# Optimization experiments

Measured on AMD Instinct MI355X. Metric: run time of the kernel, lower is better.

Reference implementation:

```python
import jax, jax.numpy as jnp
import numpy as np

HIDDEN = 2560
NUM_HEADS = 32
HEAD = HIDDEN // NUM_HEADS  # 80
ROT = 32                    # partial rotary dim (phi)
THETA = 10000.0
B, S = 2, 2048


def _apply_rope(x, pos):
    """Neox-style rotary embedding on the first ROT dims of the head.
    x: [B, S, H, HEAD], pos: [B, S] int."""
    inv_freq = 1.0 / (THETA ** (jnp.arange(0, ROT, 2, dtype=jnp.float32) / ROT))  # [ROT/2]
    freqs = pos.astype(jnp.float32)[..., None] * inv_freq  # [B, S, ROT/2]
    cos = jnp.cos(freqs)[:, :, None, :].astype(x.dtype)    # [B, S, 1, ROT/2]
    sin = jnp.sin(freqs)[:, :, None, :].astype(x.dtype)
    x_rot, x_pass = x[..., :ROT], x[..., ROT:]
    x1, x2 = x_rot[..., :ROT // 2], x_rot[..., ROT // 2:]
    rotated = jnp.concatenate([x1 * cos - x2 * sin, x2 * cos + x1 * sin], axis=-1)
    return jnp.concatenate([rotated, x_pass], axis=-1)


def setup_inputs() -> dict:
    key = jax.random.key(0)
    k0, k1, k2 = jax.random.split(key, 3)
    hidden_states = jax.random.normal(k0, (B, S, HIDDEN), dtype=jnp.float32)
    position_ids = jnp.broadcast_to(jnp.arange(S, dtype=jnp.int32), (B, S))
    Wqkv_w = jax.random.normal(k1, (3 * HIDDEN, HIDDEN), dtype=jnp.float32) * 0.02
    Wqkv_b = jnp.zeros((3 * HIDDEN,), dtype=jnp.float32)
    out_w = jax.random.normal(k2, (HIDDEN, HIDDEN), dtype=jnp.float32) * 0.02
    out_b = jnp.zeros((HIDDEN,), dtype=jnp.float32)
    return {"position_ids": position_ids, "hidden_states": hidden_states,
            "Wqkv_w": Wqkv_w, "Wqkv_b": Wqkv_b, "out_w": out_w, "out_b": out_b}


def reference(position_ids, hidden_states, Wqkv_w, Wqkv_b, out_w, out_b):
    # Fused QKV projection (torch Linear: y = x @ W^T + b)
    qkv = jnp.einsum('bsh,oh->bso', hidden_states, Wqkv_w) + Wqkv_b  # [B,S,3*HIDDEN]
    q, k, v = jnp.split(qkv, 3, axis=-1)
    q = q.reshape(B, S, NUM_HEADS, HEAD)
    k = k.reshape(B, S, NUM_HEADS, HEAD)
    v = v.reshape(B, S, NUM_HEADS, HEAD)
    # Inline RoPE on q/k (partial, first ROT dims)
    q = _apply_rope(q, position_ids)
    k = _apply_rope(k, position_ids)
    # Causal scaled-dot-product attention (math of the paged prefill kernel)
    scale = HEAD ** -0.5
    scores = jnp.einsum('bqhd,bkhd->bhqk', q, k) * scale  # [B,H,S,S]
    causal = jnp.tril(jnp.ones((S, S), dtype=bool))
    scores = jnp.where(causal, scores, jnp.finfo(scores.dtype).min)
    attn = jax.nn.softmax(scores, axis=-1)
    ctx = jnp.einsum('bhqk,bkhd->bqhd', attn, v).reshape(B, S, HIDDEN)
    return jnp.einsum('bsh,oh->bso', ctx, out_w) + out_b
```

## Files before the change

### kernel.cpp

```cpp
#include <hip/hip_runtime.h>
#include <stdint.h>

#define HIDDEN  2560
#define NHEADS  32
#define HEAD    80
#define QKS     96
#define SEQ     2048
#define BATCH   2
#define M_TOTAL (BATCH*SEQ)
#define QKV_N   (3*HIDDEN)
#define PART_SLOTS 36

typedef __attribute__((ext_vector_type(8))) short  short8;
typedef __attribute__((ext_vector_type(4))) float  floatx4;
typedef __attribute__((ext_vector_type(4))) float  fvec4;
typedef __attribute__((ext_vector_type(4))) unsigned short usvec4;
typedef __attribute__((ext_vector_type(2))) unsigned int uint2v;

#define SBAR() __builtin_amdgcn_sched_barrier(0)

__device__ __forceinline__ unsigned short f2bf(float x){
  union { float f; unsigned u; } v; v.f = x;
  unsigned r = v.u + 0x7fffu + ((v.u >> 16) & 1u);
  return (unsigned short)(r >> 16);
}
__device__ __forceinline__ float bf2f(unsigned short h){
  union { unsigned u; float f; } v; v.u = ((unsigned)h) << 16;
  return v.f;
}
__device__ __forceinline__ unsigned cvt_pk_bf16(float lo, float hi){
  unsigned r;
  asm volatile("v_cvt_pk_bf16_f32 %0, %1, %2" : "=v"(r) : "v"(lo), "v"(hi));
  return r;
}
__device__ __forceinline__ void gload16(const void* g, void* l){
  __builtin_amdgcn_global_load_lds(
    (const __attribute__((address_space(1))) void*)g,
    (__attribute__((address_space(3))) void*)l, 16, 0, 0);
}

__global__ __launch_bounds__(256)
void convert_f32_bf16(const float* __restrict__ src, unsigned short* __restrict__ dst, int n4){
  int idx = blockIdx.x*blockDim.x + threadIdx.x;
  int stride = gridDim.x*blockDim.x;
  for (int i = idx; i < n4; i += stride){
    fvec4 v = *(const fvec4*)(src + (size_t)i*4);
    usvec4 o;
    o[0]=f2bf(v[0]); o[1]=f2bf(v[1]); o[2]=f2bf(v[2]); o[3]=f2bf(v[3]);
    *(usvec4*)(dst + (size_t)i*4) = o;
  }
}

template<bool OUT_BF16>
__global__ __launch_bounds__(512, 2)
void gemm256(const unsigned short* __restrict__ A, const unsigned short* __restrict__ Bm,
             const float* __restrict__ bias, void* __restrict__ Cout,
             int M, int N, int K)
{
  __shared__ __align__(16) unsigned short lds[65536];
  const int tid  = threadIdx.x;
  const int lane = tid & 63;
  const int w    = tid >> 6;
  const int wm   = w >> 2;
  const int wn   = w & 3;
  const int l15  = lane & 15, lg = lane >> 4;

  const int gx  = gridDim.x;
  const int lid = blockIdx.y*gx + blockIdx.x;
  const int nwg = gx*gridDim.y;
  const int qch = nwg >> 3;
  const int sl  = (lid & 7)*qch + (lid >> 3);
  const int bn0 = (sl % gx) * 256;
  const int bm0 = (sl / gx) * 256;

  const int nt = K >> 6;

  int rowq[2], cq[2];
  #pragma unroll
  for (int q=0;q<2;q++){
    int u = (w*2+q)*64 + lane;
    rowq[q] = u >> 2;
    cq[q]   = ((u & 3) - (rowq[q] >> 1)) & 3;
  }
  const int rot = (lg + (l15 >> 1)) & 3;

  floatx4 acc[8][4];
  #pragma unroll
  for (int m=0;m<8;m++)
    #pragma unroll
    for (int n=0;n<4;n++) acc[m][n] = (floatx4)0.0f;

  auto STAGE = [&](int tau, int kkh){
    const int bufb = tau & 1;
    const size_t kofs = (size_t)tau*64 + kkh*32;
    const unsigned sA = (unsigned)(((bufb*2 + 0)*2 + kkh) * 8192);
    const unsigned sB = (unsigned)(((bufb*2 + 1)*2 + kkh) * 8192);
    #pragma unroll
    for (int q=0;q<2;q++){
      gload16(A  + (size_t)(bm0 + rowq[q])*K + kofs + cq[q]*8, &lds[sA + (w*2+q)*512]);
      gload16(Bm + (size_t)(bn0 + rowq[q])*K + kofs + cq[q]*8, &lds[sB + (w*2+q)*512]);
    }
  };
  auto COMPUTE = [&](int bufb, int kkh){
    const unsigned short* As = &lds[((bufb*2+0)*2+kkh)*8192];
    const unsigned short* Bs = &lds[((bufb*2+1)*2+kkh)*8192];
    short8 af[8], bfv[4];
    __builtin_amdgcn_s_setprio(1);
    #pragma unroll
    for (int n=0;n<4;n++)
      bfv[n] = *(const short8*)&Bs[(((wn*64 + n*16 + l15)<<2) + rot)*8];
    #pragma unroll
    for (int m=0;m<8;m++)
      af[m] = *(const short8*)&As[(((wm*128 + m*16 + l15)<<2) + rot)*8];
    #pragma unroll
    for (int m=0;m<8;m++)
      #pragma unroll
      for (int n=0;n<4;n++)
        acc[m][n] = __builtin_amdgcn_mfma_f32_16x16x32_bf16(af[m], bfv[n], acc[m][n], 0, 0, 0);
    __builtin_amdgcn_s_setprio(0);
  };

  STAGE(0,0);
  STAGE(0,1);
  STAGE(1,0);
  asm volatile("s_waitcnt vmcnt(8)" ::: "memory");
  __builtin_amdgcn_s_barrier(); SBAR();

  for (int t=0; t<nt; ++t){
    const int c = t & 1;
    if (t+1 < nt) STAGE(t+1, 1);
    COMPUTE(c, 0);
    if (t+1 < nt) asm volatile("s_waitcnt vmcnt(8)" ::: "memory");
    else          asm volatile("s_waitcnt vmcnt(0)" ::: "memory");
    __builtin_amdgcn_s_barrier(); SBAR();
    if (t+2 < nt) STAGE(t+2, 0);
    COMPUTE(c, 1);
    if (t+1 < nt){
      if (t+2 < nt) asm volatile("s_waitcnt vmcnt(8)" ::: "memory");
      else          asm volatile("s_waitcnt vmcnt(4)" ::: "memory");
      __builtin_amdgcn_s_barrier(); SBAR();
    }
  }

  #pragma unroll
  for (int m=0;m<8;m++){
    #pragma unroll
    for (int n=0;n<4;n++){
      int col = bn0 + wn*64 + n*16 + l15;
      float bs = bias[col];
      #pragma unroll
      for (int r=0;r<4;r++){
        int row = bm0 + wm*128 + m*16 + lg*4 + r;
        float v = acc[m][n][r] + bs;
        if (OUT_BF16) ((unsigned short*)Cout)[(size_t)row*N + col] = f2bf(v);
        else          ((float*)Cout)[(size_t)row*N + col] = v;
      }
    }
  }
}

__global__ __launch_bounds__(256)
void rope_scatter(const unsigned short* __restrict__ qkv,
                  const int* __restrict__ pos_ids,
                  unsigned short* __restrict__ Qp, unsigned short* __restrict__ Kp,
                  unsigned short* __restrict__ Vt)
{
  __shared__ float cosb[128*16];
  __shared__ float sinb[128*16];
  __shared__ __align__(16) unsigned short vtile[128*88];
  const int tid = threadIdx.x;
  const int blk = blockIdx.x;
  const int st = blk & 15, h = (blk >> 4) & 31, b = blk >> 9;
  const int s0 = st*128;

  for (int idx = tid; idx < 128*16; idx += 256){
    int sl = idx >> 4, i = idx & 15;
    float p = (float)pos_ids[b*SEQ + s0 + sl];
    float inv = exp2f(-(float)i * (13.287712379549449f/16.0f));
    float ang = p * inv;
    cosb[idx] = cosf(ang);
    sinb[idx] = sinf(ang);
  }
  __syncthreads();

  const size_t qkrow = (size_t)(b*SEQ + s0)*QKV_N;
  const size_t obase = ((size_t)(b*NHEADS + h)*SEQ + s0)*QKS;
  #pragma unroll
  for (int part = 0; part < 2; part++){
    const int cbase = part*HIDDEN + h*HEAD;
    unsigned short* outp = part ? Kp : Qp;
    for (int idx = tid; idx < 128*QKS; idx += 256){
      int sl = idx / QKS, d = idx - sl*QKS;
      const size_t rb = qkrow + (size_t)sl*QKV_N + cbase;
      float v;
      if (d < 16){
        float x1 = bf2f(qkv[rb + d]);
        float x2 = bf2f(qkv[rb + d + 16]);
        v = x1*cosb[sl*16 + d] - x2*sinb[sl*16 + d];
      } else if (d < 32){
        int i = d - 16;
        float x1 = bf2f(qkv[rb + d - 16]);
        float x2 = bf2f(qkv[rb + d]);
        v = x2*cosb[sl*16 + i] + x1*sinb[sl*16 + i];
      } else if (d < HEAD){
        v = bf2f(qkv[rb + d]);
      } else v = 0.0f;
      outp[obase + (size_t)sl*QKS + d] = f2bf(v);
    }
  }

  for (int idx = tid; idx < 128*HEAD; idx += 256){
    int sl = idx / HEAD, d = idx - sl*HEAD;
    vtile[sl*88 + d] = qkv[qkrow + (size_t)sl*QKV_N + 2*HIDDEN + h*HEAD + d];
  }
  __syncthreads();
  const size_t vtb = ((size_t)(b*NHEADS + h)*HEAD)*SEQ + s0;
  for (int idx = tid; idx < HEAD*128; idx += 256){
    int d = idx >> 7, sl = idx & 127;
    Vt[vtb + (size_t)d*SEQ + sl] = vtile[sl*88 + d];
  }
}

__global__ __launch_bounds__(256, 4)
void attn_fd(const unsigned short* __restrict__ Qp,
             const unsigned short* __restrict__ Kp,
             const unsigned short* __restrict__ Vt,
             unsigned short* __restrict__ ctx,
             unsigned short* __restrict__ pO,
             float* __restrict__ pML)
{
  __shared__ __align__(16) unsigned short Klds[64*96];
  __shared__ __align__(16) unsigned short Vlds[80*64];
  __shared__ __align__(16) unsigned short p_lds[4][32*36];
  const int tid = threadIdx.x;
  const int lane = tid & 63, w = tid >> 6;
  const int l15 = lane & 15, lg = lane >> 4;

  const int bid = blockIdx.x;
  const int xcd = bid & 7, j = bid >> 3;
  const int bh  = (j/40)*8 + xcd;
  const int tr  = j - (j/40)*40;

  int qt, part, np;
  if (tr < 16)      { qt = 12 + (tr>>2); part = tr & 3; np = 4; }
  else if (tr < 28) { int t = tr-16; int q3 = t/3; qt = 8 + q3; part = t - q3*3; np = 3; }
  else if (tr < 36) { int t = tr-28; qt = 4 + (t>>1); part = t & 1; np = 2; }
  else              { qt = tr - 36; part = 0; np = 1; }
  const int nk  = 2*qt + 2;
  const int kt0 = (part*nk)/np, kt1 = ((part+1)*nk)/np;
  const int q0  = qt*128 + w*32;

  const unsigned short* Qb = Qp + ((size_t)bh*SEQ)*QKS;
  const unsigned short* Kb = Kp + ((size_t)bh*SEQ)*QKS;
  const unsigned short* Vb = Vt + ((size_t)bh*HEAD)*SEQ;

  short8 qf[2][3];
  #pragma unroll
  for (int mi=0; mi<2; mi++)
    #pragma unroll
    for (int kc=0; kc<3; kc++)
      qf[mi][kc] = *(const short8*)&Qb[(size_t)(q0 + mi*16 + l15)*QKS + kc*32 + lg*8];

  int ksrow[3], ksc[3];
  #pragma unroll
  for (int t=0;t<3;t++){
    int ci = (w*3 + t)*64 + lane;
    int row = ci/12, c = ci - row*12;
    ksrow[t] = row;
    ksc[t]   = (c ^ (row & 3))*8;
  }
  int vsrow[3], vsc[3];
  #pragma unroll
  for (int t=0;t<3;t++){
    int i = w + 4*t;
    int row = i*8 + (lane >> 3), c = lane & 7;
    vsrow[t] = row;
    vsc[t]   = (c ^ (row & 7))*8;
  }

  float mrun[2] = {-3e38f, -3e38f};
  float lrun[2] = {0.0f, 0.0f};
  floatx4 oacc[2][5];
  #pragma unroll
  for (int mi=0;mi<2;mi++)
    #pragma unroll
    for (int di=0;di<5;di++) oacc[mi][di] = (floatx4)0.0f;

  const float SC = 0.1118033988749895f * 1.4426950408889634f;

  for (int kt = kt0; kt < kt1; kt++){
    #pragma unroll
    for (int t=0;t<3;t++)
      gload16(Kb + (size_t)(kt*64 + ksrow[t])*QKS + ksc[t], &Klds[(w*3+t)*512]);
    #pragma unroll
    for (int t=0;t<3;t++){
      int i = w + 4*t;
      if (i < 10)
        gload16(Vb + (size_t)vsrow[t]*SEQ + kt*64 + vsc[t], &Vlds[i*512]);
    }
    __syncthreads();

    if (kt*64 <= q0 + 31){
      floatx4 sacc[2][4];
      #pragma unroll
      for (int mi=0;mi<2;mi++)
        #pragma unroll
        for (int ni=0;ni<4;ni++) sacc[mi][ni] = (floatx4)0.0f;

      __builtin_amdgcn_s_setprio(1);
      #pragma unroll
      for (int kc=0; kc<3; kc++){
        short8 kf[4];
        #pragma unroll
        for (int ni=0; ni<4; ni++){
          int r = ni*16 + l15;
          kf[ni] = *(const short8*)&Klds[r*96 + (((kc*4+lg) ^ (r & 3))<<3)];
        }
        #pragma unroll
        for (int mi=0; mi<2; mi++)
          #pragma unroll
          for (int ni=0; ni<4; ni++)
            sacc[mi][ni] = __builtin_amdgcn_mfma_f32_16x16x32_bf16(kf[ni], qf[mi][kc], sacc[mi][ni], 0, 0, 0);
      }
      __builtin_amdgcn_s_setprio(0);

      if (kt*64 + 63 > q0){
        #pragma unroll
        for (int mi=0; mi<2; mi++){
          int qrow = q0 + mi*16 + l15;
          #pragma unroll
          for (int ni=0; ni<4; ni++){
            int kb = kt*64 + ni*16 + lg*4;
            #pragma unroll
            for (int r=0; r<4; r++)
              if (kb + r > qrow) sacc[mi][ni][r] = -3e38f;
          }
        }
      }

      #pragma unroll
      for (int mi=0; mi<2; mi++){
        float pm = -3e38f;
        #pragma unroll
        for (int ni=0; ni<4; ni++)
          #pragma unroll
          for (int r=0; r<4; r++) pm = fmaxf(pm, sacc[mi][ni][r]);
        pm = fmaxf(pm, __shfl_xor(pm, 16));
        pm = fmaxf(pm, __shfl_xor(pm, 32));
        float mold = mrun[mi];
        float mnew = fmaxf(mold, pm);
        float msc  = mnew*SC;
        float alpha = __builtin_amdgcn_exp2f(mold*SC - msc);
        float rs = 0.0f;
        #pragma unroll
        for (int ni=0; ni<4; ni++)
          #pragma unroll
          for (int r=0; r<4; r++){
            float p = __builtin_amdgcn_exp2f(sacc[mi][ni][r]*SC - msc);
            sacc[mi][ni][r] = p;
            rs += p;
          }
        rs += __shfl_xor(rs, 16);
        rs += __shfl_xor(rs, 32);
        lrun[mi] = lrun[mi]*alpha + rs;
        mrun[mi] = mnew;
        #pragma unroll
        for (int di=0; di<5; di++) oacc[mi][di] *= alpha;
      }

      #pragma unroll
      for (int kk=0; kk<2; kk++){
        #pragma unroll
        for (int mi=0; mi<2; mi++)
          #pragma unroll
          for (int nl=0; nl<2; nl++){
            int ni = kk*2 + nl;
            uint2v pk;
            pk[0] = cvt_pk_bf16(sacc[mi][ni][0], sacc[mi][ni][1]);
            pk[1] = cvt_pk_bf16(sacc[mi][ni][2], sacc[mi][ni][3]);
            *(uint2v*)&p_lds[w][(mi*16 + l15)*36 + nl*16 + lg*4] = pk;
          }
        __builtin_amdgcn_s_setprio(1);
        short8 pa[2];
        #pragma unroll
        for (int mi=0;mi<2;mi++)
          pa[mi] = *(const short8*)&p_lds[w][(mi*16 + l15)*36 + lg*8];
        #pragma unroll
        for (int di=0; di<5; di++){
          int r = di*16 + l15;
          short8 vf = *(const short8*)&Vlds[r*64 + (((kk*4+lg) ^ (r & 7))<<3)];
          #pragma unroll
          for (int mi=0;mi<2;mi++)
            oacc[mi][di] = __builtin_amdgcn_mfma_f32_16x16x32_bf16(vf, pa[mi], oacc[mi][di], 0, 0, 0);
        }
        __builtin_amdgcn_s_setprio(0);
      }
    }
    __syncthreads();
  }

  const int b = bh >> 5, h = bh & 31;
  if (np == 1){
    #pragma unroll
    for (int mi=0;mi<2;mi++){
      float inv = 1.0f/lrun[mi];
      size_t crow = ((size_t)(b*SEQ + q0 + mi*16 + l15))*HIDDEN + h*HEAD;
      #pragma unroll
      for (int di=0;di<5;di++){
        uint2v pk;
        pk[0] = cvt_pk_bf16(oacc[mi][di][0]*inv, oacc[mi][di][1]*inv);
        pk[1] = cvt_pk_bf16(oacc[mi][di][2]*inv, oacc[mi][di][3]*inv);
        *(uint2v*)&ctx[crow + di*16 + lg*4] = pk;
      }
    }
  } else {
    int base;
    if (np == 2)      base = (qt-4)*2;
    else if (np == 3) base = 8 + (qt-8)*3;
    else              base = 20 + (qt-12)*4;
    const int pslot = bh*PART_SLOTS + base + part;
    unsigned short* Ob = pO + (size_t)pslot*128*HEAD;
    #pragma unroll
    for (int mi=0;mi<2;mi++){
      int grow = w*32 + mi*16 + l15;
      #pragma unroll
      for (int di=0;di<5;di++){
        uint2v pk;
        pk[0] = cvt_pk_bf16(oacc[mi][di][0], oacc[mi][di][1]);
        pk[1] = cvt_pk_bf16(oacc[mi][di][2], oacc[mi][di][3]);
        *(uint2v*)&Ob[grow*HEAD + di*16 + lg*4] = pk;
      }
      if (lg == 0){
        float* mlb = pML + ((size_t)pslot*128 + grow)*2;
        mlb[0] = mrun[mi];
        mlb[1] = lrun[mi];
      }
    }
  }
}

__global__ __launch_bounds__(256)
void attn_combine(const unsigned short* __restrict__ pO, const float* __restrict__ pML,
                  unsigned short* __restrict__ ctx)
{
  const int bid = blockIdx.x;
  const int bh = bid / 12, qt = 4 + (bid - (bid/12)*12);
  int base, np;
  if (qt < 8)       { base = (qt-4)*2;       np = 2; }
  else if (qt < 12) { base = 8 + (qt-8)*3;   np = 3; }
  else              { base = 20 + (qt-12)*4; np = 4; }
  const int slot0 = bh*PART_SLOTS + base;
  const float SC = 0.1118033988749895f * 1.4426950408889634f;
  const int b = bh >> 5, h = bh & 31;

  #pragma unroll
  for (int c = 0; c < 5; c++){
    const int e   = c*2048 + threadIdx.x*8;
    const int row = e / 80, d = e - row*80;

    float m[4], l[4], ms = -3e38f;
    for (int p=0;p<np;p++){
      const float* mlb = pML + ((size_t)(slot0+p)*128 + row)*2;
      m[p] = mlb[0]; l[p] = mlb[1];
      ms = fmaxf(ms, m[p]);
    }
    float wgt[4], lsum = 0.0f;
    for (int p=0;p<np;p++){
      wgt[p] = exp2f((m[p]-ms)*SC);
      lsum += wgt[p]*l[p];
    }
    const float inv = 1.0f/lsum;

    float acc[8] = {0,0,0,0,0,0,0,0};
    for (int p=0;p<np;p++){
      short8 v = *(const short8*)&pO[(size_t)(slot0+p)*128*HEAD + e];
      #pragma unroll
      for (int j=0;j<8;j++) acc[j] += wgt[p]*bf2f((unsigned short)v[j]);
    }
    short8 o;
    #pragma unroll
    for (int j=0;j<8;j++) o[j] = (short)f2bf(acc[j]*inv);
    *(short8*)&ctx[((size_t)(b*SEQ + qt*128 + row))*HIDDEN + h*HEAD + d] = o;
  }
}

extern "C" void kernel_launch(void* const* d_in, const int* in_sizes, int n_in,
                              void* d_out, int out_size, void* d_ws, size_t ws_size,
                              hipStream_t stream)
{
  const int*   pos  = (const int*)  d_in[0];
  const float* hid  = (const float*)d_in[1];
  const float* wqkv = (const float*)d_in[2];
  const float* bqkv = (const float*)d_in[3];
  const float* outw = (const float*)d_in[4];
  const float* outb = (const float*)d_in[5];

  char* ws = (char*)d_ws;
  size_t off = 0;
  auto alloc = [&](size_t bytes)->void*{
    void* p = ws + off; off += (bytes + 255) & ~(size_t)255; return p;
  };
  unsigned short* hid_bf  = (unsigned short*)alloc((size_t)M_TOTAL*HIDDEN*2);
  unsigned short* wqkv_bf = (unsigned short*)alloc((size_t)QKV_N*HIDDEN*2);
  unsigned short* outw_bf = (unsigned short*)alloc((size_t)HIDDEN*HIDDEN*2);
  unsigned short* qkv_bf  = (unsigned short*)alloc((size_t)M_TOTAL*QKV_N*2);
  unsigned short* Qp      = (unsigned short*)alloc((size_t)BATCH*NHEADS*SEQ*QKS*2);
  unsigned short* Kp      = (unsigned short*)alloc((size_t)BATCH*NHEADS*SEQ*QKS*2);
  unsigned short* Vt      = (unsigned short*)alloc((size_t)BATCH*NHEADS*HEAD*SEQ*2);
  if (off > ws_size) return;

  unsigned short* pO  = qkv_bf;
  float*          pML = (float*)(qkv_bf + (size_t)64*PART_SLOTS*128*HEAD);

  convert_f32_bf16<<<dim3(1024), dim3(256), 0, stream>>>(hid,  hid_bf,  M_TOTAL*HIDDEN/4);
  convert_f32_bf16<<<dim3(2048), dim3(256), 0, stream>>>(wqkv, wqkv_bf, QKV_N*HIDDEN/4);
  convert_f32_bf16<<<dim3(1024), dim3(256), 0, stream>>>(outw, outw_bf, HIDDEN*HIDDEN/4);

  gemm256<true><<<dim3(QKV_N/256, M_TOTAL/256), dim3(512), 0, stream>>>(
      hid_bf, wqkv_bf, bqkv, (void*)qkv_bf, M_TOTAL, QKV_N, HIDDEN);

  rope_scatter<<<dim3(BATCH*NHEADS*16), dim3(256), 0, stream>>>(qkv_bf, pos, Qp, Kp, Vt);

  unsigned short* ctx = hid_bf;
  attn_fd<<<dim3(2560), dim3(256), 0, stream>>>(Qp, Kp, Vt, ctx, pO, pML);
  attn_combine<<<dim3(64*12), dim3(256), 0, stream>>>(pO, pML, ctx);

  gemm256<false><<<dim3(HIDDEN/256, M_TOTAL/256), dim3(512), 0, stream>>>(
      ctx, outw_bf, outb, d_out, M_TOTAL, HIDDEN, HIDDEN);
}
```

Before: 545.0 us.

## Restructure GEMM main loop into four-phase ping-pong with per-unit staging

```diff
diff --git a/kernel.cpp b/kernel.cpp
--- a/kernel.cpp
+++ b/kernel.cpp
@@ -74,6 +74,7 @@
   const int bm0 = (sl / gx) * 256;
 
   const int nt = K >> 6;
+  const int NU = nt*4;
 
   int rowq[2], cq[2];
   #pragma unroll
@@ -90,55 +91,60 @@
     #pragma unroll
     for (int n=0;n<4;n++) acc[m][n] = (floatx4)0.0f;
 
-  auto STAGE = [&](int tau, int kkh){
-    const int bufb = tau & 1;
+  auto STAGE_UNIT = [&](int u){
+    const int tau = u >> 2, j = u & 3;
+    const int mat = j & 1;
+    const int kkh = j >> 1;
+    const unsigned base = (unsigned)(((((tau & 1)*2 + mat)*2) + kkh) * 8192);
+    const unsigned short* src = mat ? Bm : A;
+    const int r0 = mat ? bn0 : bm0;
     const size_t kofs = (size_t)tau*64 + kkh*32;
-    const unsigned sA = (unsigned)(((bufb*2 + 0)*2 + kkh) * 8192);
-    const unsigned sB = (unsigned)(((bufb*2 + 1)*2 + kkh) * 8192);
-    #pragma unroll
-    for (int q=0;q<2;q++){
-      gload16(A  + (size_t)(bm0 + rowq[q])*K + kofs + cq[q]*8, &lds[sA + (w*2+q)*512]);
-      gload16(Bm + (size_t)(bn0 + rowq[q])*K + kofs + cq[q]*8, &lds[sB + (w*2+q)*512]);
-    }
+    #pragma unroll
+    for (int q=0;q<2;q++)
+      gload16(src + (size_t)(r0 + rowq[q])*K + kofs + cq[q]*8, &lds[base + (w*2+q)*512]);
   };
-  auto COMPUTE = [&](int bufb, int kkh){
-    const unsigned short* As = &lds[((bufb*2+0)*2+kkh)*8192];
+
+  short8 af[4], bfv[4];
+  auto READ_B = [&](int bufb, int kkh){
     const unsigned short* Bs = &lds[((bufb*2+1)*2+kkh)*8192];
-    short8 af[8], bfv[4];
-    __builtin_amdgcn_s_setprio(1);
     #pragma unroll
     for (int n=0;n<4;n++)
       bfv[n] = *(const short8*)&Bs[(((wn*64 + n*16 + l15)<<2) + rot)*8];
-    #pragma unroll
-    for (int m=0;m<8;m++)
-      af[m] = *(const short8*)&As[(((wm*128 + m*16 + l15)<<2) + rot)*8];
-    #pragma unroll
-    for (int m=0;m<8;m++)
-      #pragma unroll
-      for (int n=0;n<4;n++)
-        acc[m][n] = __builtin_amdgcn_mfma_f32_16x16x32_bf16(af[m], bfv[n], acc[m][n], 0, 0, 0);
-    __builtin_amdgcn_s_setprio(0);
   };
-
-  STAGE(0,0);
-  STAGE(0,1);
-  STAGE(1,0);
-  asm volatile("s_waitcnt vmcnt(8)" ::: "memory");
-  __builtin_amdgcn_s_barrier(); SBAR();
+  auto READ_A = [&](int bufb, int kkh, int mh){
+    const unsigned short* As = &lds[((bufb*2+0)*2+kkh)*8192];
+    #pragma unroll
+    for (int m=0;m<4;m++)
+      af[m] = *(const short8*)&As[(((wm*128 + (mh*4+m)*16 + l15)<<2) + rot)*8];
+  };
+
+  int u = 0;
+  for (; u < 6 && u < NU; ++u) STAGE_UNIT(u);
+  if (NU > 6) asm volatile("s_waitcnt vmcnt(4)" ::: "memory");
+  else        asm volatile("s_waitcnt vmcnt(0)" ::: "memory");
+  SBAR(); __builtin_amdgcn_s_barrier(); SBAR();
 
   for (int t=0; t<nt; ++t){
     const int c = t & 1;
-    if (t+1 < nt) STAGE(t+1, 1);
-    COMPUTE(c, 0);
-    if (t+1 < nt) asm volatile("s_waitcnt vmcnt(8)" ::: "memory");
-    else          asm volatile("s_waitcnt vmcnt(0)" ::: "memory");
-    __builtin_amdgcn_s_barrier(); SBAR();
-    if (t+2 < nt) STAGE(t+2, 0);
-    COMPUTE(c, 1);
-    if (t+1 < nt){
-      if (t+2 < nt) asm volatile("s_waitcnt vmcnt(8)" ::: "memory");
-      else          asm volatile("s_waitcnt vmcnt(4)" ::: "memory");
-      __builtin_amdgcn_s_barrier(); SBAR();
+    #pragma unroll
+    for (int ph=0; ph<4; ++ph){
+      const int kkh = ph >> 1, mh = ph & 1;
+      if (mh == 0) READ_B(c, kkh);
+      READ_A(c, kkh, mh);
+      if (u < NU){ STAGE_UNIT(u); ++u; }
+      if (ph == 3){
+        if (t < nt-2)       asm volatile("s_waitcnt vmcnt(4)" ::: "memory");
+        else if (t == nt-2) asm volatile("s_waitcnt vmcnt(0)" ::: "memory");
+      }
+      SBAR(); __builtin_amdgcn_s_barrier(); SBAR();
+      __builtin_amdgcn_s_setprio(1);
+      #pragma unroll
+      for (int m=0;m<4;m++)
+        #pragma unroll
+        for (int n=0;n<4;n++)
+          acc[mh*4+m][n] = __builtin_amdgcn_mfma_f32_16x16x32_bf16(af[m], bfv[n], acc[mh*4+m][n], 0, 0, 0);
+      __builtin_amdgcn_s_setprio(0);
+      SBAR(); __builtin_amdgcn_s_barrier(); SBAR();
     }
   }
 
```

New measurement: 567.0 us (median of 2 runs). 4.0% more time.
